# Kernel optimization log

Hardware: AMD Instinct MI355X
Metric: run time of the kernel (lower is better)

The kernel has to match this reference:

```python
import jax, jax.numpy as jnp
import numpy as np

EPS = 1e-12  # torch F.normalize default eps

def l2norm(x, axis):
    n = jnp.sqrt(jnp.sum(x * x, axis=axis, keepdims=True))
    return x / jnp.maximum(n, EPS)

def conv2d(x, w, b, pad):
    y = jax.lax.conv_general_dilated(x, w, (1, 1), [(pad, pad), (pad, pad)],
                                     dimension_numbers=('NCHW', 'OIHW', 'NCHW'))
    return y + b[None, :, None, None]

def setup_inputs() -> dict:
    key = jax.random.key(0)
    ks = jax.random.split(key, 12)
    N, C, H, W, K = 16, 256, 64, 64, 32
    s = 0.05
    return {
        'feature':   jax.random.normal(ks[0], (N, C, H, W), jnp.float32),
        'conv_up_w': jax.random.normal(ks[1], (K, C, 3, 3), jnp.float32) * s,
        'conv_up_b': jax.random.normal(ks[2], (K,), jnp.float32) * s,
        'centroids': jax.random.uniform(ks[3], (K, C), jnp.float32),
        'upfc_w':    jax.random.normal(ks[4], (C, K * C), jnp.float32) * s,
        'upfc_b':    jax.random.normal(ks[5], (C,), jnp.float32) * s,
        't1_w':      jax.random.normal(ks[6], (C, 2 * C, 1, 1), jnp.float32) * s,
        't1_b':      jax.random.normal(ks[7], (C,), jnp.float32) * s,
        't2_w':      jax.random.normal(ks[8], (C, C, 1, 1), jnp.float32) * s,
        't2_b':      jax.random.normal(ks[9], (C,), jnp.float32) * s,
    }

def reference(feature, conv_up_w, conv_up_b, centroids, upfc_w, upfc_b, t1_w, t1_b, t2_w, t2_b):
    N, C, H, W = feature.shape
    K = centroids.shape[0]
    # --- UP branch ---
    xn = l2norm(feature, axis=1)                       # (N,C,H,W)
    sa = jax.nn.softmax(conv2d(xn, conv_up_w, conv_up_b, 1), axis=1)  # (N,K,H,W)
    sa_flat = sa.reshape(N, K, H * W)                  # (N,K,L)
    x_flat = xn.reshape(N, C, H * W)                   # (N,C,L)
    # sum_l sa[n,k,l] * (x[n,c,l] - centroid[k,c])  ==  two matmuls, no (N,K,C,L) tensor
    up = jnp.einsum('nkl,ncl->nkc', sa_flat, x_flat) \
         - jnp.sum(sa_flat, axis=-1)[:, :, None] * centroids[None]   # (N,K,C)
    up = l2norm(up, axis=2).reshape(N, K * C)
    up = l2norm(up, axis=1)
    up = up @ upfc_w.T + upfc_b                        # (N,C)
    up_map = jnp.broadcast_to(up[:, :, None, None], (N, C, H, W))
    # --- transform ---
    nf = jnp.concatenate([feature, up_map], axis=1)    # (N,2C,H,W)
    h = jax.nn.relu(conv2d(nf, t1_w, t1_b, 0))
    return jax.nn.relu(conv2d(h, t2_w, t2_b, 0))
```

## Files before the change

kernel.cpp:

```cpp
#include <hip/hip_runtime.h>
#include <cstdint>

#define N_ 16
#define C_ 256
#define H_ 64
#define W_ 64
#define L_ 4096
#define K_ 32
#define CL_ (C_*L_)
#define KL_ (K_*L_)
#define KC_ (K_*C_)

typedef __attribute__((ext_vector_type(8))) short short8;
typedef __attribute__((ext_vector_type(4))) float f32x4;

__device__ __forceinline__ unsigned short f2bf(float x) {
    unsigned int u = __float_as_uint(x);
    u += 0x7fffu + ((u >> 16) & 1u);
    return (unsigned short)(u >> 16);
}
__device__ __forceinline__ unsigned int pack2(float a, float b) {
    return (unsigned int)f2bf(a) | ((unsigned int)f2bf(b) << 16);
}

__device__ __forceinline__ void glds16(const void* g, void* l) {
    __builtin_amdgcn_global_load_lds(
        (const __attribute__((address_space(1))) unsigned int*)g,
        (__attribute__((address_space(3))) unsigned int*)l, 16, 0, 0);
}

__global__ __launch_bounds__(256) void k_prep(
    const float* __restrict__ f, float* __restrict__ rinv,
    unsigned short* __restrict__ xnb)
{
    __shared__ float tile[256 * 34];
    __shared__ float ssred[8 * 33];
    __shared__ float rbuf[32];
    int bid = blockIdx.x;
    int n = bid >> 7;
    int l0 = (bid & 127) << 5;
    int tid = threadIdx.x;
    int l = tid & 31, cb = tid >> 5;
    const float* fp = f + (size_t)n * CL_ + l0 + l;
    float ss = 0.f;
#pragma unroll
    for (int i = 0; i < 32; ++i) {
        int c = (cb << 5) + i;
        float v = fp[(size_t)c * L_];
        tile[c * 34 + l] = v;
        ss = fmaf(v, v, ss);
    }
    ssred[cb * 33 + l] = ss;
    __syncthreads();
    if (tid < 32) {
        float s = 0.f;
#pragma unroll
        for (int j = 0; j < 8; ++j) s += ssred[j * 33 + tid];
        float ri = 1.0f / fmaxf(sqrtf(s), 1e-12f);
        rinv[n * L_ + l0 + tid] = ri;
        rbuf[tid] = ri;
    }
    __syncthreads();
    float ri = rbuf[l];
    unsigned short* op = xnb + ((size_t)n * L_ + l0 + l) * C_ + (cb << 5);
#pragma unroll
    for (int g = 0; g < 4; ++g) {
        unsigned int pk[4];
#pragma unroll
        for (int d = 0; d < 4; ++d) {
            int c = (cb << 5) + (g << 3) + (d << 1);
            pk[d] = pack2(tile[c * 34 + l] * ri, tile[(c + 1) * 34 + l] * ri);
        }
        *(uint4*)(op + (g << 3)) = make_uint4(pk[0], pk[1], pk[2], pk[3]);
    }
}

__global__ __launch_bounds__(256) void k_wpack(const float* __restrict__ w, unsigned short* __restrict__ wb) {
    int i = blockIdx.x * 256 + threadIdx.x;
    int j = i & 7;
    int k = (i >> 3) & 31;
    int q = (i >> 8) & 3;
    int ch = (i >> 10) & 7;
    int t = i >> 13;
    int c = (ch << 5) + (q << 3) + j;
    wb[i] = f2bf(w[k * 2304 + c * 9 + t]);
}

__global__ __launch_bounds__(256) void k_wpackp(const float* __restrict__ w, int stride,
                                                unsigned short* __restrict__ wb2) {
    int i = blockIdx.x * 256 + threadIdx.x;
    int j = i & 7, co = (i >> 3) & 255, q = (i >> 11) & 3, ch = i >> 13;
    int ci = (ch << 5) + (q << 3) + j;
    wb2[i] = f2bf(w[(size_t)co * stride + ci]);
}

__global__ __launch_bounds__(128, 2) void k_conv(
    const unsigned short* __restrict__ xnb, const unsigned short* __restrict__ wb,
    const float* __restrict__ bias, const float* __restrict__ zpad,
    float* __restrict__ sa, float* __restrict__ ssum)
{
    __shared__ __align__(16) unsigned short lsB[2][408 * 8];
    __shared__ __align__(16) unsigned short lsW[2][1152 * 8];
    __shared__ float sred[2][32];
    int bid = blockIdx.x;
    int n = bid & 15, y = (bid >> 4) & 63, px_b = bid >> 10;
    int tid = threadIdx.x;
    int wv = tid >> 6, lane = tid & 63;
    int r = lane & 15, quad = lane >> 4;
    int pxw = (wv << 4) + r;
    int xbase = (px_b << 5) - 1;
    const unsigned short* xb = xnb + (size_t)n * CL_;
    const unsigned short* zp = (const unsigned short*)zpad;

    const unsigned short* bsrc[4];
    bool bact[4];
#pragma unroll
    for (int k = 0; k < 4; ++k) {
        int c = (wv << 6) + (k << 7) + lane;
        bool act = c < 408;
        int cc = act ? c : 0;
        int row = cc / 136;
        int rem = cc - row * 136;
        int q = rem / 34;
        int px = rem - q * 34;
        int yy = y + row - 1, xx = xbase + px;
        bool ok = act && ((unsigned)yy < 64u) && ((unsigned)xx < 64u);
        bsrc[k] = ok ? (xb + (((size_t)(yy << 6) + xx) << 8) + (q << 3)) : zp;
        bact[k] = act;
    }

    f32x4 acc0 = (f32x4){0.f, 0.f, 0.f, 0.f};
    f32x4 acc1 = (f32x4){0.f, 0.f, 0.f, 0.f};

    {
#pragma unroll
        for (int k = 0; k < 4; ++k)
            if (bact[k]) glds16(bsrc[k], lsB[0] + (((wv << 6) + (k << 7)) << 3));
#pragma unroll
        for (int k = 0; k < 9; ++k) {
            int idx = wv * 9 + k;
            int t = idx >> 1, h = idx & 1;
            glds16(wb + (t << 13) + (h << 9) + (lane << 3), lsW[0] + (idx << 9));
        }
    }

    for (int i = 0; i < 8; ++i) {
        asm volatile("s_waitcnt vmcnt(0)" ::: "memory");
        __syncthreads();
        if (i < 7) {
            int c1 = (i + 1) << 5;
            unsigned short* dB = lsB[(i + 1) & 1];
            unsigned short* dW = lsW[(i + 1) & 1];
#pragma unroll
            for (int k = 0; k < 4; ++k)
                if (bact[k]) glds16(bsrc[k] + c1, dB + (((wv << 6) + (k << 7)) << 3));
#pragma unroll
            for (int k = 0; k < 9; ++k) {
                int idx = wv * 9 + k;
                int t = idx >> 1, h = idx & 1;
                glds16(wb + (t << 13) + (h << 9) + ((i + 1) << 10) + (lane << 3),
                       dW + (idx << 9));
            }
        }
        const unsigned short* bufB = lsB[i & 1];
        const unsigned short* bufW = lsW[i & 1];
#pragma unroll
        for (int dy = 0; dy < 3; ++dy) {
#pragma unroll
            for (int dx = 0; dx < 3; ++dx) {
                int t = dy * 3 + dx;
                short8 B  = *(const short8*)(bufB + ((((dy << 2) + quad) * 34 + (pxw + dx)) << 3));
                short8 A0 = *(const short8*)(bufW + (((t << 7) + (quad << 5) + r) << 3));
                short8 A1 = *(const short8*)(bufW + (((t << 7) + (quad << 5) + 16 + r) << 3));
                acc0 = __builtin_amdgcn_mfma_f32_16x16x32_bf16(A0, B, acc0, 0, 0, 0);
                acc1 = __builtin_amdgcn_mfma_f32_16x16x32_bf16(A1, B, acc1, 0, 0, 0);
            }
        }
    }
    float4 b0 = *(const float4*)(bias + (quad << 2));
    float4 b1 = *(const float4*)(bias + 16 + (quad << 2));
    float v[8];
    v[0] = acc0[0] + b0.x; v[1] = acc0[1] + b0.y; v[2] = acc0[2] + b0.z; v[3] = acc0[3] + b0.w;
    v[4] = acc1[0] + b1.x; v[5] = acc1[1] + b1.y; v[6] = acc1[2] + b1.z; v[7] = acc1[3] + b1.w;
    float mx = v[0];
#pragma unroll
    for (int j = 1; j < 8; ++j) mx = fmaxf(mx, v[j]);
    mx = fmaxf(mx, __shfl_xor(mx, 16));
    mx = fmaxf(mx, __shfl_xor(mx, 32));
    float s = 0.f;
#pragma unroll
    for (int j = 0; j < 8; ++j) { v[j] = __expf(v[j] - mx); s += v[j]; }
    s += __shfl_xor(s, 16);
    s += __shfl_xor(s, 32);
    float rs = 1.0f / s;
    float sv8[8];
#pragma unroll
    for (int j = 0; j < 8; ++j) sv8[j] = v[j] * rs;
    int l = (y << 6) + (px_b << 5) + pxw;
    float* sp = sa + (size_t)n * KL_ + l;
#pragma unroll
    for (int j = 0; j < 4; ++j) {
        sp[(size_t)((quad << 2) + j) * L_] = sv8[j];
        sp[(size_t)(16 + (quad << 2) + j) * L_] = sv8[4 + j];
    }
#pragma unroll
    for (int j = 0; j < 8; ++j) {
        float a = sv8[j];
        a += __shfl_xor(a, 1); a += __shfl_xor(a, 2);
        a += __shfl_xor(a, 4); a += __shfl_xor(a, 8);
        sv8[j] = a;
    }
    if (r == 0) {
#pragma unroll
        for (int j = 0; j < 4; ++j) {
            sred[wv][(quad << 2) + j] = sv8[j];
            sred[wv][16 + (quad << 2) + j] = sv8[4 + j];
        }
    }
    __syncthreads();
    if (tid < 32) {
        float t = sred[0][tid] + sred[1][tid];
        atomicAdd(ssum + n * K_ + tid, t);
    }
}

__global__ __launch_bounds__(256) void k_einsum(
    const float* __restrict__ f, const float* __restrict__ rinv,
    const float* __restrict__ sa, float* __restrict__ up)
{
    __shared__ float xn_s[C_ * 33];
    __shared__ float sa_s[K_ * 32];
    int bid = blockIdx.x;
    int n = bid >> 5;
    int l0 = (bid & 31) << 7;
    int tid = threadIdx.x;
    int kq = tid >> 5, cq = tid & 31;
    float acc[4][8];
#pragma unroll
    for (int i = 0; i < 4; ++i)
#pragma unroll
        for (int j = 0; j < 8; ++j) acc[i][j] = 0.f;

    for (int ch = 0; ch < 4; ++ch) {
        int lc = l0 + (ch << 5);
        __syncthreads();
        {
            int crow = tid >> 3, lq = (tid & 7) << 2;
#pragma unroll
            for (int p = 0; p < 8; ++p) {
                int c = (p << 5) + crow;
                float4 f4 = *(const float4*)(f + (size_t)n * CL_ + (size_t)c * L_ + lc + lq);
                float4 r4 = *(const float4*)(rinv + n * L_ + lc + lq);
                float* d = xn_s + c * 33 + lq;
                d[0] = f4.x * r4.x; d[1] = f4.y * r4.y; d[2] = f4.z * r4.z; d[3] = f4.w * r4.w;
            }
        }
        {
            int k = tid >> 3, lq = (tid & 7) << 2;
            float4 a4 = *(const float4*)(sa + (size_t)n * KL_ + (size_t)k * L_ + lc + lq);
            *(float4*)(sa_s + (k << 5) + lq) = a4;
        }
        __syncthreads();
#pragma unroll 4
        for (int l = 0; l < 32; ++l) {
            float sv[4], xv[8];
#pragma unroll
            for (int i = 0; i < 4; ++i) sv[i] = sa_s[((kq << 2) + i) * 32 + l];
#pragma unroll
            for (int j = 0; j < 8; ++j) xv[j] = xn_s[(cq + (j << 5)) * 33 + l];
#pragma unroll
            for (int i = 0; i < 4; ++i)
#pragma unroll
                for (int j = 0; j < 8; ++j) acc[i][j] = fmaf(sv[i], xv[j], acc[i][j]);
        }
    }
    float* upp = up + (size_t)n * KC_;
#pragma unroll
    for (int i = 0; i < 4; ++i)
#pragma unroll
        for (int j = 0; j < 8; ++j)
            atomicAdd(upp + ((kq << 2) + i) * C_ + cq + (j << 5), acc[i][j]);
}

__global__ __launch_bounds__(256) void k_rowfix(
    const float* __restrict__ up, const float* __restrict__ ssum,
    const float* __restrict__ cent, float* __restrict__ upn, float* __restrict__ rowss)
{
    __shared__ float red[256];
    int bid = blockIdx.x;
    int k = bid & 31;
    float sv = ssum[bid];
    float v = up[(size_t)bid * C_ + threadIdx.x] - sv * cent[k * C_ + threadIdx.x];
    red[threadIdx.x] = v * v; __syncthreads();
    for (int st = 128; st > 0; st >>= 1) {
        if (threadIdx.x < st) red[threadIdx.x] += red[threadIdx.x + st];
        __syncthreads();
    }
    float ss = red[0];
    float ri = 1.0f / fmaxf(sqrtf(ss), 1e-12f);
    upn[(size_t)bid * C_ + threadIdx.x] = v * ri;
    if (threadIdx.x == 0) rowss[bid] = ss * ri * ri;
}

__global__ __launch_bounds__(256) void k_fc(
    const float* __restrict__ upn, const float* __restrict__ rowss,
    const float* __restrict__ w, const float* __restrict__ b,
    float* __restrict__ upvec)
{
    __shared__ float rnb[16];
    __shared__ float red[16][5];
    int c = blockIdx.x;
    int tid = threadIdx.x;
    int wv = tid >> 6, lane = tid & 63;
    if (tid < 16) {
        float ts = 0.f;
#pragma unroll
        for (int k = 0; k < K_; ++k) ts += rowss[(tid << 5) + k];
        rnb[tid] = 1.0f / fmaxf(sqrtf(ts), 1e-12f);
    }
    float acc[16];
#pragma unroll
    for (int n = 0; n < 16; ++n) acc[n] = 0.f;
    const float* wr = w + (size_t)c * KC_;
#pragma unroll
    for (int g = 0; g < 8; ++g) {
        int kc = (g << 10) + (tid << 2);
        float4 w4 = *(const float4*)(wr + kc);
#pragma unroll
        for (int n = 0; n < 16; ++n) {
            float4 u4 = *(const float4*)(upn + n * KC_ + kc);
            acc[n] += w4.x * u4.x + w4.y * u4.y + w4.z * u4.z + w4.w * u4.w;
        }
    }
#pragma unroll
    for (int n = 0; n < 16; ++n) {
        float a = acc[n];
#pragma unroll
        for (int s = 1; s < 64; s <<= 1) a += __shfl_xor(a, s);
        if (lane == 0) red[n][wv] = a;
    }
    __syncthreads();
    if (tid < 16) {
        float v = red[tid][0] + red[tid][1] + red[tid][2] + red[tid][3];
        upvec[tid * C_ + c] = v * rnb[tid] + b[c];
    }
}

__global__ __launch_bounds__(256) void k_t1up(
    const float* __restrict__ upvec, const float* __restrict__ t1w,
    const float* __restrict__ t1b, float* __restrict__ t1up)
{
    __shared__ float wld[256];
    int co = blockIdx.x;
    int tid = threadIdx.x;
    wld[tid] = t1w[(size_t)co * 512 + 256 + tid];
    __syncthreads();
    int n = tid >> 4, s = tid & 15;
    float a = 0.f;
#pragma unroll
    for (int i = 0; i < 16; ++i)
        a += wld[s + (i << 4)] * upvec[n * C_ + s + (i << 4)];
#pragma unroll
    for (int st = 1; st < 16; st <<= 1) a += __shfl_xor(a, st);
    if (s == 0) t1up[n * C_ + co] = a + t1b[co];
}

__global__ __launch_bounds__(256) void k_gemm1(
    const float* __restrict__ f, const unsigned short* __restrict__ wb2,
    const float* __restrict__ t1up, unsigned short* __restrict__ hb)
{
    __shared__ __align__(16) unsigned int lsB[2][128 * 20];
    __shared__ __align__(16) unsigned short lsW[2][512 * 8];
    int bid = blockIdx.x;
    int co_b = bid & 1, px_b = (bid >> 1) & 31, n = bid >> 6;
    int l0 = px_b << 7;
    int tid = threadIdx.x;
    int wv = tid >> 6, lane = tid & 63;
    int r = lane & 15, quad = lane >> 4;
    int pxl = (wv >> 1) << 6;
    int co0l = (wv & 1) << 6;
    int co0 = (co_b << 7) + co0l;
    const float* fb_ = f + (size_t)n * CL_ + l0;
    int c2 = tid & 15, pxg = tid >> 4;

    float4 ra[2], rb[2];
#pragma unroll
    for (int k2 = 0; k2 < 2; ++k2) {
        const float* s0 = fb_ + (size_t)(c2 << 1) * L_ + ((pxg + (k2 << 4)) << 2);
        ra[k2] = *(const float4*)s0;
        rb[k2] = *(const float4*)(s0 + L_);
    }
#pragma unroll
    for (int k = 0; k < 2; ++k)
        glds16(wb2 + (((wv << 8) + (co_b << 7) + (k << 6) + lane) << 3),
               lsW[0] + (((wv << 7) + (k << 6)) << 3));

    f32x4 acc[4][4];
#pragma unroll
    for (int i = 0; i < 4; ++i)
#pragma unroll
        for (int j = 0; j < 4; ++j) acc[i][j] = (f32x4){0.f, 0.f, 0.f, 0.f};

    for (int i = 0; i < 8; ++i) {
        unsigned int* buf = lsB[i & 1];
        unsigned int pk[2][4];
#pragma unroll
        for (int k2 = 0; k2 < 2; ++k2) {
            pk[k2][0] = pack2(ra[k2].x, rb[k2].x); pk[k2][1] = pack2(ra[k2].y, rb[k2].y);
            pk[k2][2] = pack2(ra[k2].z, rb[k2].z); pk[k2][3] = pack2(ra[k2].w, rb[k2].w);
        }
#pragma unroll
        for (int k2 = 0; k2 < 2; ++k2) {
            int base = (pxg + (k2 << 4)) * 80 + c2;
            buf[base]      = pk[k2][0];
            buf[base + 20] = pk[k2][1];
            buf[base + 40] = pk[k2][2];
            buf[base + 60] = pk[k2][3];
        }
        asm volatile("s_waitcnt vmcnt(0)" ::: "memory");
        __syncthreads();
        if (i < 7) {
#pragma unroll
            for (int k2 = 0; k2 < 2; ++k2) {
                const float* s0 = fb_ + (size_t)(((i + 1) << 5) + (c2 << 1)) * L_ + ((pxg + (k2 << 4)) << 2);
                ra[k2] = *(const float4*)s0;
                rb[k2] = *(const float4*)(s0 + L_);
            }
#pragma unroll
            for (int k = 0; k < 2; ++k)
                glds16(wb2 + ((((((i + 1) << 2) + wv) << 8) + (co_b << 7) + (k << 6) + lane) << 3),
                       lsW[(i + 1) & 1] + (((wv << 7) + (k << 6)) << 3));
        }
        const unsigned short* bufW = lsW[i & 1];
        short8 A[4], B[4];
#pragma unroll
        for (int t = 0; t < 4; ++t)
            A[t] = *(const short8*)(bufW + (((quad << 7) + co0l + (t << 4) + r) << 3));
#pragma unroll
        for (int t = 0; t < 4; ++t)
            B[t] = *(const short8*)((const unsigned short*)buf + (pxl + (t << 4) + r) * 40 + (quad << 3));
#pragma unroll
        for (int pxt = 0; pxt < 4; ++pxt)
#pragma unroll
            for (int cot = 0; cot < 4; ++cot)
                acc[pxt][cot] = __builtin_amdgcn_mfma_f32_16x16x32_bf16(A[cot], B[pxt], acc[pxt][cot], 0, 0, 0);
    }
#pragma unroll
    for (int pxt = 0; pxt < 4; ++pxt) {
        int px = l0 + pxl + (pxt << 4) + r;
        unsigned short* orow = hb + ((size_t)n * L_ + px) * C_;
#pragma unroll
        for (int cot = 0; cot < 4; ++cot) {
            int cb = co0 + (cot << 4) + (quad << 2);
            float4 bb = *(const float4*)(t1up + n * C_ + cb);
            unsigned int p0 = pack2(fmaxf(acc[pxt][cot][0] + bb.x, 0.f),
                                    fmaxf(acc[pxt][cot][1] + bb.y, 0.f));
            unsigned int p1 = pack2(fmaxf(acc[pxt][cot][2] + bb.z, 0.f),
                                    fmaxf(acc[pxt][cot][3] + bb.w, 0.f));
            *(uint2*)(orow + cb) = make_uint2(p0, p1);
        }
    }
}

__global__ __launch_bounds__(256) void k_gemm2(
    const unsigned short* __restrict__ hb, const unsigned short* __restrict__ wb2,
    const float* __restrict__ t2b, float* __restrict__ out)
{
    __shared__ __align__(16) unsigned short lsB[2][512 * 8];
    __shared__ __align__(16) unsigned short lsW[2][512 * 8];
    int bid = blockIdx.x;
    int co_b = bid & 1, px_b = (bid >> 1) & 31, n = bid >> 6;
    int l0 = px_b << 7;
    int tid = threadIdx.x;
    int wv = tid >> 6, lane = tid & 63;
    int r = lane & 15, quad = lane >> 4;
    int pxl = (wv >> 1) << 6;
    int co0l = (wv & 1) << 6;
    int co0 = (co_b << 7) + co0l;
    const unsigned short* hrow = hb + ((size_t)n * L_ + l0) * C_;

#pragma unroll
    for (int k = 0; k < 2; ++k) {
        glds16(hrow + (size_t)((k << 6) + lane) * C_ + (wv << 3),
               lsB[0] + (((wv << 7) + (k << 6)) << 3));
        glds16(wb2 + (((wv << 8) + (co_b << 7) + (k << 6) + lane) << 3),
               lsW[0] + (((wv << 7) + (k << 6)) << 3));
    }

    f32x4 acc[4][4];
#pragma unroll
    for (int i = 0; i < 4; ++i)
#pragma unroll
        for (int j = 0; j < 4; ++j) acc[i][j] = (f32x4){0.f, 0.f, 0.f, 0.f};

    for (int i = 0; i < 8; ++i) {
        asm volatile("s_waitcnt vmcnt(0)" ::: "memory");
        __syncthreads();
        if (i < 7) {
#pragma unroll
            for (int k = 0; k < 2; ++k) {
                glds16(hrow + (size_t)((k << 6) + lane) * C_ + ((i + 1) << 5) + (wv << 3),
                       lsB[(i + 1) & 1] + (((wv << 7) + (k << 6)) << 3));
                glds16(wb2 + ((((((i + 1) << 2) + wv) << 8) + (co_b << 7) + (k << 6) + lane) << 3),
                       lsW[(i + 1) & 1] + (((wv << 7) + (k << 6)) << 3));
            }
        }
        const unsigned short* bufB = lsB[i & 1];
        const unsigned short* bufW = lsW[i & 1];
        short8 A[4], B[4];
#pragma unroll
        for (int t = 0; t < 4; ++t)
            A[t] = *(const short8*)(bufW + (((quad << 7) + co0l + (t << 4) + r) << 3));
#pragma unroll
        for (int t = 0; t < 4; ++t)
            B[t] = *(const short8*)(bufB + (((quad << 7) + pxl + (t << 4) + r) << 3));
#pragma unroll
        for (int pxt = 0; pxt < 4; ++pxt)
#pragma unroll
            for (int cot = 0; cot < 4; ++cot)
                acc[pxt][cot] = __builtin_amdgcn_mfma_f32_16x16x32_bf16(A[cot], B[pxt], acc[pxt][cot], 0, 0, 0);
    }
#pragma unroll
    for (int pxt = 0; pxt < 4; ++pxt) {
        int px = l0 + pxl + (pxt << 4) + r;
#pragma unroll
        for (int cot = 0; cot < 4; ++cot) {
            int cb = co0 + (cot << 4) + (quad << 2);
            float4 bb = *(const float4*)(t2b + cb);
            out[((size_t)n * C_ + cb + 0) * L_ + px] = fmaxf(acc[pxt][cot][0] + bb.x, 0.f);
            out[((size_t)n * C_ + cb + 1) * L_ + px] = fmaxf(acc[pxt][cot][1] + bb.y, 0.f);
            out[((size_t)n * C_ + cb + 2) * L_ + px] = fmaxf(acc[pxt][cot][2] + bb.z, 0.f);
            out[((size_t)n * C_ + cb + 3) * L_ + px] = fmaxf(acc[pxt][cot][3] + bb.w, 0.f);
        }
    }
}

extern "C" void kernel_launch(void* const* d_in, const int* in_sizes, int n_in,
                              void* d_out, int out_size, void* d_ws, size_t ws_size,
                              hipStream_t stream)
{
    const float* feature = (const float*)d_in[0];
    const float* conv_w  = (const float*)d_in[1];
    const float* conv_b  = (const float*)d_in[2];
    const float* cent    = (const float*)d_in[3];
    const float* upfc_w  = (const float*)d_in[4];
    const float* upfc_b  = (const float*)d_in[5];
    const float* t1w     = (const float*)d_in[6];
    const float* t1b     = (const float*)d_in[7];
    const float* t2w     = (const float*)d_in[8];
    const float* t2b     = (const float*)d_in[9];

    float* ws = (float*)d_ws;
    unsigned short* xnb = (unsigned short*)ws;
    unsigned short* hb  = xnb;
    float* rest  = ws + 8388608;
    float* rinv  = rest;
    float* sa    = rinv + 65536;
    float* up    = sa + 2097152;
    float* ssum  = up + 131072;
    float* zpad  = ssum + 512;
    float* upn   = zpad + 512;
    float* rowss = upn + 131072;
    float* upvec = rowss + 512;
    float* t1up  = upvec + 4096;
    unsigned short* wbconv = (unsigned short*)upn;
    unsigned short* t1wb = (unsigned short*)sa;
    unsigned short* t2wb = t1wb + 65536;
    float* out = (float*)d_out;

    hipMemsetAsync(up, 0, (131072 + 512 + 512) * sizeof(float), stream);
    k_prep     <<<2048, 256, 0, stream>>>(feature, rinv, xnb);
    k_wpack    <<<288,  256, 0, stream>>>(conv_w, wbconv);
    k_conv     <<<2048, 128, 0, stream>>>(xnb, wbconv, conv_b, zpad, sa, ssum);
    k_einsum   <<<512,  256, 0, stream>>>(feature, rinv, sa, up);
    k_rowfix   <<<512,  256, 0, stream>>>(up, ssum, cent, upn, rowss);
    k_wpackp   <<<256,  256, 0, stream>>>(t1w, 512, t1wb);
    k_wpackp   <<<256,  256, 0, stream>>>(t2w, 256, t2wb);
    k_fc       <<<256,  256, 0, stream>>>(upn, rowss, upfc_w, upfc_b, upvec);
    k_t1up     <<<256,  256, 0, stream>>>(upvec, t1w, t1b, t1up);
    k_gemm1    <<<1024, 256, 0, stream>>>(feature, t1wb, t1up, hb);
    k_gemm2    <<<1024, 256, 0, stream>>>(hb, t2wb, t2b, out);
}
```

Before: 299.8 us.

## Feed first transform GEMM from bf16 normalized features and rescale by norm

```diff
diff --git a/kernel.cpp b/kernel.cpp
--- a/kernel.cpp
+++ b/kernel.cpp
@@ -31,7 +31,7 @@
 
 __global__ __launch_bounds__(256) void k_prep(
     const float* __restrict__ f, float* __restrict__ rinv,
-    unsigned short* __restrict__ xnb)
+    float* __restrict__ snorm, unsigned short* __restrict__ xnb)
 {
     __shared__ float tile[256 * 34];
     __shared__ float ssred[8 * 33];
@@ -56,8 +56,10 @@
         float s = 0.f;
 #pragma unroll
         for (int j = 0; j < 8; ++j) s += ssred[j * 33 + tid];
-        float ri = 1.0f / fmaxf(sqrtf(s), 1e-12f);
+        float sq = fmaxf(sqrtf(s), 1e-12f);
+        float ri = 1.0f / sq;
         rinv[n * L_ + l0 + tid] = ri;
+        snorm[n * L_ + l0 + tid] = sq;
         rbuf[tid] = ri;
     }
     __syncthreads();
@@ -365,35 +367,33 @@
     if (s == 0) t1up[n * C_ + co] = a + t1b[co];
 }
 
-__global__ __launch_bounds__(256) void k_gemm1(
-    const float* __restrict__ f, const unsigned short* __restrict__ wb2,
-    const float* __restrict__ t1up, unsigned short* __restrict__ hb)
-{
-    __shared__ __align__(16) unsigned int lsB[2][128 * 20];
-    __shared__ __align__(16) unsigned short lsW[2][512 * 8];
+__global__ __launch_bounds__(512, 2) void k_gemm1(
+    const unsigned short* __restrict__ xnb, const unsigned short* __restrict__ wb2,
+    const float* __restrict__ t1up, const float* __restrict__ snorm,
+    unsigned short* __restrict__ hb)
+{
+    __shared__ __align__(16) unsigned short lsB[2][512 * 8];
+    __shared__ __align__(16) unsigned short lsW[2][1024 * 8];
     int bid = blockIdx.x;
-    int co_b = bid & 1, px_b = (bid >> 1) & 31, n = bid >> 6;
+    int n = bid & 15, px_b = bid >> 4;
     int l0 = px_b << 7;
     int tid = threadIdx.x;
     int wv = tid >> 6, lane = tid & 63;
     int r = lane & 15, quad = lane >> 4;
-    int pxl = (wv >> 1) << 6;
-    int co0l = (wv & 1) << 6;
-    int co0 = (co_b << 7) + co0l;
-    const float* fb_ = f + (size_t)n * CL_ + l0;
-    int c2 = tid & 15, pxg = tid >> 4;
-
-    float4 ra[2], rb[2];
-#pragma unroll
-    for (int k2 = 0; k2 < 2; ++k2) {
-        const float* s0 = fb_ + (size_t)(c2 << 1) * L_ + ((pxg + (k2 << 4)) << 2);
-        ra[k2] = *(const float4*)s0;
-        rb[k2] = *(const float4*)(s0 + L_);
-    }
-#pragma unroll
-    for (int k = 0; k < 2; ++k)
-        glds16(wb2 + (((wv << 8) + (co_b << 7) + (k << 6) + lane) << 3),
-               lsW[0] + (((wv << 7) + (k << 6)) << 3));
+    int pxl = (wv >> 2) << 6;
+    int co0 = (wv & 3) << 6;
+    const unsigned short* xrow = xnb + ((size_t)n * L_ + l0) * C_;
+
+    int cbi = (wv << 6) + lane;
+    int bq = cbi >> 7, bpx = cbi & 127;
+    const unsigned short* bsrc = xrow + (size_t)bpx * C_ + (bq << 3);
+
+    glds16(bsrc, lsB[0] + (cbi << 3));
+#pragma unroll
+    for (int k = 0; k < 2; ++k) {
+        int cw = (wv << 7) + (k << 6) + lane;
+        glds16(wb2 + ((size_t)cw << 3), lsW[0] + (cw << 3));
+    }
 
     f32x4 acc[4][4];
 #pragma unroll
@@ -402,43 +402,26 @@
         for (int j = 0; j < 4; ++j) acc[i][j] = (f32x4){0.f, 0.f, 0.f, 0.f};
 
     for (int i = 0; i < 8; ++i) {
-        unsigned int* buf = lsB[i & 1];
-        unsigned int pk[2][4];
-#pragma unroll
-        for (int k2 = 0; k2 < 2; ++k2) {
-            pk[k2][0] = pack2(ra[k2].x, rb[k2].x); pk[k2][1] = pack2(ra[k2].y, rb[k2].y);
-            pk[k2][2] = pack2(ra[k2].z, rb[k2].z); pk[k2][3] = pack2(ra[k2].w, rb[k2].w);
-        }
-#pragma unroll
-        for (int k2 = 0; k2 < 2; ++k2) {
-            int base = (pxg + (k2 << 4)) * 80 + c2;
-            buf[base]      = pk[k2][0];
-            buf[base + 20] = pk[k2][1];
-            buf[base + 40] = pk[k2][2];
-            buf[base + 60] = pk[k2][3];
-        }
         asm volatile("s_waitcnt vmcnt(0)" ::: "memory");
         __syncthreads();
         if (i < 7) {
-#pragma unroll
-            for (int k2 = 0; k2 < 2; ++k2) {
-                const float* s0 = fb_ + (size_t)(((i + 1) << 5) + (c2 << 1)) * L_ + ((pxg + (k2 << 4)) << 2);
-                ra[k2] = *(const float4*)s0;
-                rb[k2] = *(const float4*)(s0 + L_);
+            glds16(bsrc + ((i + 1) << 5), lsB[(i + 1) & 1] + (cbi << 3));
+#pragma unroll
+            for (int k = 0; k < 2; ++k) {
+                int cw = (wv << 7) + (k << 6) + lane;
+                glds16(wb2 + ((size_t)(((i + 1) << 10) + cw) << 3),
+                       lsW[(i + 1) & 1] + (cw << 3));
             }
-#pragma unroll
-            for (int k = 0; k < 2; ++k)
-                glds16(wb2 + ((((((i + 1) << 2) + wv) << 8) + (co_b << 7) + (k << 6) + lane) << 3),
-                       lsW[(i + 1) & 1] + (((wv << 7) + (k << 6)) << 3));
-        }
+        }
+        const unsigned short* bufB = lsB[i & 1];
         const unsigned short* bufW = lsW[i & 1];
         short8 A[4], B[4];
 #pragma unroll
         for (int t = 0; t < 4; ++t)
-            A[t] = *(const short8*)(bufW + (((quad << 7) + co0l + (t << 4) + r) << 3));
+            A[t] = *(const short8*)(bufW + (((quad << 8) + co0 + (t << 4) + r) << 3));
 #pragma unroll
         for (int t = 0; t < 4; ++t)
-            B[t] = *(const short8*)((const unsigned short*)buf + (pxl + (t << 4) + r) * 40 + (quad << 3));
+            B[t] = *(const short8*)(bufB + (((quad << 7) + pxl + (t << 4) + r) << 3));
 #pragma unroll
         for (int pxt = 0; pxt < 4; ++pxt)
 #pragma unroll
@@ -448,15 +431,16 @@
 #pragma unroll
     for (int pxt = 0; pxt < 4; ++pxt) {
         int px = l0 + pxl + (pxt << 4) + r;
+        float sc = snorm[n * L_ + px];
         unsigned short* orow = hb + ((size_t)n * L_ + px) * C_;
 #pragma unroll
         for (int cot = 0; cot < 4; ++cot) {
             int cb = co0 + (cot << 4) + (quad << 2);
             float4 bb = *(const float4*)(t1up + n * C_ + cb);
-            unsigned int p0 = pack2(fmaxf(acc[pxt][cot][0] + bb.x, 0.f),
-                                    fmaxf(acc[pxt][cot][1] + bb.y, 0.f));
-            unsigned int p1 = pack2(fmaxf(acc[pxt][cot][2] + bb.z, 0.f),
-                                    fmaxf(acc[pxt][cot][3] + bb.w, 0.f));
+            unsigned int p0 = pack2(fmaxf(fmaf(acc[pxt][cot][0], sc, bb.x), 0.f),
+                                    fmaxf(fmaf(acc[pxt][cot][1], sc, bb.y), 0.f));
+            unsigned int p1 = pack2(fmaxf(fmaf(acc[pxt][cot][2], sc, bb.z), 0.f),
+                                    fmaxf(fmaf(acc[pxt][cot][3], sc, bb.w), 0.f));
             *(uint2*)(orow + cb) = make_uint2(p0, p1);
         }
     }
@@ -559,7 +543,8 @@
     float* up    = sa + 2097152;
     float* ssum  = up + 131072;
     float* zpad  = ssum + 512;
-    float* upn   = zpad + 512;
+    float* snorm = zpad + 512;
+    float* upn   = snorm + 65536;
     float* rowss = upn + 131072;
     float* upvec = rowss + 512;
     float* t1up  = upvec + 4096;
@@ -569,7 +554,7 @@
     float* out = (float*)d_out;
 
     hipMemsetAsync(up, 0, (131072 + 512 + 512) * sizeof(float), stream);
-    k_prep     <<<2048, 256, 0, stream>>>(feature, rinv, xnb);
+    k_prep     <<<2048, 256, 0, stream>>>(feature, rinv, snorm, xnb);
     k_wpack    <<<288,  256, 0, stream>>>(conv_w, wbconv);
     k_conv     <<<2048, 128, 0, stream>>>(xnb, wbconv, conv_b, zpad, sa, ssum);
     k_einsum   <<<512,  256, 0, stream>>>(feature, rinv, sa, up);
@@ -578,6 +563,6 @@
     k_wpackp   <<<256,  256, 0, stream>>>(t2w, 256, t2wb);
     k_fc       <<<256,  256, 0, stream>>>(upn, rowss, upfc_w, upfc_b, upvec);
     k_t1up     <<<256,  256, 0, stream>>>(upvec, t1w, t1b, t1up);
-    k_gemm1    <<<1024, 256, 0, stream>>>(feature, t1wb, t1up, hb);
+    k_gemm1    <<<512,  512, 0, stream>>>(xnb, t1wb, t1up, snorm, hb);
     k_gemm2    <<<1024, 256, 0, stream>>>(hb, t2wb, t2b, out);
 }
```

New measurement: 285.8 us. 4.7% less time.
